# Performance work log

Hardware: AMD Instinct MI355X
Metric: run time of the kernel (lower is better)

Reference implementation:

```python
import jax, jax.numpy as jnp
import numpy as np
import math

B, T, D = 16, 4, 1024
H = 16
DH = D // H  # 64
S = 8192  # kv cache length


def setup_inputs() -> dict:
    key = jax.random.key(0)
    ks = jax.random.split(key, 5)
    return {
        "x": jax.random.normal(ks[0], (B, T, D), dtype=jnp.float32),
        "cache_k": jax.random.normal(ks[1], (B, S, H, DH), dtype=jnp.float32),
        "cache_v": jax.random.normal(ks[2], (B, S, H, DH), dtype=jnp.float32),
        "w_qkv": jax.random.normal(ks[3], (3 * D, D), dtype=jnp.float32) * 0.02,
        "w_proj": jax.random.normal(ks[4], (D, D), dtype=jnp.float32) * (0.02 / math.sqrt(24)),
    }


def reference(x, cache_k, cache_v, w_qkv, w_proj):
    # QKV projection: [B,T,3D]
    qkv = jnp.einsum('btd,ed->bte', x, w_qkv)
    q, k, v = jnp.split(qkv, 3, axis=-1)
    q = q.reshape(B, T, H, DH)
    k = k.reshape(B, T, H, DH)
    v = v.reshape(B, T, H, DH)
    # KV cache concat along sequence dim
    k = jnp.concatenate([cache_k, k], axis=1)  # [B,S+T,H,DH]
    v = jnp.concatenate([cache_v, v], axis=1)
    # scaled dot-product attention (no mask, dropout=0)
    scores = jnp.einsum('bthd,bshd->bhts', q, k) / math.sqrt(DH)
    attn = jax.nn.softmax(scores.astype(jnp.float32), axis=-1).astype(q.dtype)
    out = jnp.einsum('bhts,bshd->bthd', attn, v).reshape(B, T, D)
    # output projection
    out = jnp.einsum('btd,ed->bte', out, w_proj)
    return out
```

## Files before the change

### kernel.cpp

```cpp
#include <hip/hip_runtime.h>
#include <math.h>

#define B_ 16
#define T_ 4
#define D_ 1024
#define H_ 16
#define DH_ 64
#define S_ 8192
#define NW 8
#define ROWS_PER_WAVE (S_ / NW)
#define UNROLL 4

__device__ __forceinline__ void online_step(const float4* q4, const float4& kf,
                                            const float4& vf, float* m, float* l,
                                            float4* o) {
  float sc[T_];
#pragma unroll
  for (int t = 0; t < T_; ++t)
    sc[t] = q4[t].x * kf.x + q4[t].y * kf.y + q4[t].z * kf.z + q4[t].w * kf.w;
#pragma unroll
  for (int mask = 1; mask < 16; mask <<= 1) {
#pragma unroll
    for (int t = 0; t < T_; ++t) sc[t] += __shfl_xor(sc[t], mask);
  }
#pragma unroll
  for (int t = 0; t < T_; ++t) {
    float s = sc[t] * 0.125f;
    float nm = fmaxf(m[t], s);
    float al = __expf(m[t] - nm);
    float p = __expf(s - nm);
    m[t] = nm;
    l[t] = fmaf(l[t], al, p);
    o[t].x = fmaf(o[t].x, al, p * vf.x);
    o[t].y = fmaf(o[t].y, al, p * vf.y);
    o[t].z = fmaf(o[t].z, al, p * vf.z);
    o[t].w = fmaf(o[t].w, al, p * vf.w);
  }
}

__device__ __forceinline__ void merge_xor(int mask, float* m, float* l, float4* o) {
#pragma unroll
  for (int t = 0; t < T_; ++t) {
    float om = __shfl_xor(m[t], mask);
    float ol = __shfl_xor(l[t], mask);
    float4 oo;
    oo.x = __shfl_xor(o[t].x, mask);
    oo.y = __shfl_xor(o[t].y, mask);
    oo.z = __shfl_xor(o[t].z, mask);
    oo.w = __shfl_xor(o[t].w, mask);
    float nm = fmaxf(m[t], om);
    float ea = __expf(m[t] - nm);
    float eb = __expf(om - nm);
    m[t] = nm;
    l[t] = l[t] * ea + ol * eb;
    o[t].x = o[t].x * ea + oo.x * eb;
    o[t].y = o[t].y * ea + oo.y * eb;
    o[t].z = o[t].z * ea + oo.z * eb;
    o[t].w = o[t].w * ea + oo.w * eb;
  }
}

__global__ __launch_bounds__(NW * 64) void attn_kernel(
    const float* __restrict__ qkv, const float* __restrict__ cache_k,
    const float* __restrict__ cache_v, float* __restrict__ attn_out) {
  const int bh = blockIdx.x;
  const int b = bh >> 4;
  const int h = bh & 15;
  const int tid = threadIdx.x;
  const int wave = tid >> 6;
  const int lane = tid & 63;
  const int s_sub = lane >> 4;
  const int d4 = lane & 15;

  float4 q4[T_];
#pragma unroll
  for (int t = 0; t < T_; ++t)
    q4[t] = *(const float4*)(qkv + (size_t)((b * T_ + t) * 3 * D_ + h * DH_ + d4 * 4));

  const float* kbase = cache_k + (size_t)b * S_ * D_ + h * DH_ + d4 * 4;
  const float* vbase = cache_v + (size_t)b * S_ * D_ + h * DH_ + d4 * 4;

  float m[T_], l[T_];
  float4 o[T_];
#pragma unroll
  for (int t = 0; t < T_; ++t) {
    m[t] = -1e30f;
    l[t] = 0.f;
    o[t] = make_float4(0.f, 0.f, 0.f, 0.f);
  }

  const int row0 = wave * ROWS_PER_WAVE + s_sub;
  for (int it = 0; it < ROWS_PER_WAVE / (4 * UNROLL); ++it) {
    const float* kp = kbase + (size_t)(row0 + it * 4 * UNROLL) * D_;
    const float* vp = vbase + (size_t)(row0 + it * 4 * UNROLL) * D_;
    float4 kf[UNROLL], vf[UNROLL];
#pragma unroll
    for (int u = 0; u < UNROLL; ++u) {
      kf[u] = *(const float4*)(kp + (size_t)u * 4 * D_);
      vf[u] = *(const float4*)(vp + (size_t)u * 4 * D_);
    }
#pragma unroll
    for (int u = 0; u < UNROLL; ++u) online_step(q4, kf[u], vf[u], m, l, o);
  }

  if (wave == 0) {
    const float* krow = qkv + (size_t)((b * T_ + s_sub) * 3 * D_ + D_ + h * DH_ + d4 * 4);
    const float* vrow = qkv + (size_t)((b * T_ + s_sub) * 3 * D_ + 2 * D_ + h * DH_ + d4 * 4);
    float4 kf = *(const float4*)krow;
    float4 vf = *(const float4*)vrow;
    online_step(q4, kf, vf, m, l, o);
  }

  merge_xor(16, m, l, o);
  merge_xor(32, m, l, o);

  __shared__ float lm[NW][T_];
  __shared__ float ll[NW][T_];
  __shared__ float lo[NW][T_][DH_];
  if (lane < 16) {
#pragma unroll
    for (int t = 0; t < T_; ++t) {
      if (lane == 0) {
        lm[wave][t] = m[t];
        ll[wave][t] = l[t];
      }
      *(float4*)(&lo[wave][t][lane * 4]) = o[t];
    }
  }
  __syncthreads();
  if (tid < DH_) {
    const int d = tid;
#pragma unroll
    for (int t = 0; t < T_; ++t) {
      float M = -1e30f;
#pragma unroll
      for (int w = 0; w < NW; ++w) M = fmaxf(M, lm[w][t]);
      float L = 0.f, O = 0.f;
#pragma unroll
      for (int w = 0; w < NW; ++w) {
        float e = __expf(lm[w][t] - M);
        L += ll[w][t] * e;
        O += lo[w][t][d] * e;
      }
      attn_out[(size_t)(b * T_ + t) * D_ + h * DH_ + d] = O / L;
    }
  }
}

__global__ __launch_bounds__(256) void gemm_xwt(const float* __restrict__ A,
                                                const float* __restrict__ W,
                                                float* __restrict__ C, int N) {
  const int K = 1024;
  __shared__ float As[32][65];
  __shared__ float Bs[32][65];
  const int tid = threadIdx.x;
  const int n0 = blockIdx.x * 64;
  const int tx = tid & 15;
  const int ty = tid >> 4;
  const int lrow = tid >> 2;
  const int lk = (tid & 3) * 8;

  float acc[4][4] = {};
  for (int k0 = 0; k0 < K; k0 += 32) {
    float4 a0 = *(const float4*)(A + (size_t)lrow * K + k0 + lk);
    float4 a1 = *(const float4*)(A + (size_t)lrow * K + k0 + lk + 4);
    float4 b0 = *(const float4*)(W + (size_t)(n0 + lrow) * K + k0 + lk);
    float4 b1 = *(const float4*)(W + (size_t)(n0 + lrow) * K + k0 + lk + 4);
    As[lk + 0][lrow] = a0.x; As[lk + 1][lrow] = a0.y;
    As[lk + 2][lrow] = a0.z; As[lk + 3][lrow] = a0.w;
    As[lk + 4][lrow] = a1.x; As[lk + 5][lrow] = a1.y;
    As[lk + 6][lrow] = a1.z; As[lk + 7][lrow] = a1.w;
    Bs[lk + 0][lrow] = b0.x; Bs[lk + 1][lrow] = b0.y;
    Bs[lk + 2][lrow] = b0.z; Bs[lk + 3][lrow] = b0.w;
    Bs[lk + 4][lrow] = b1.x; Bs[lk + 5][lrow] = b1.y;
    Bs[lk + 6][lrow] = b1.z; Bs[lk + 7][lrow] = b1.w;
    __syncthreads();
#pragma unroll
    for (int kk = 0; kk < 32; ++kk) {
      float a[4], bb[4];
#pragma unroll
      for (int i = 0; i < 4; ++i) a[i] = As[kk][ty * 4 + i];
#pragma unroll
      for (int j = 0; j < 4; ++j) bb[j] = Bs[kk][tx * 4 + j];
#pragma unroll
      for (int i = 0; i < 4; ++i)
#pragma unroll
        for (int j = 0; j < 4; ++j) acc[i][j] = fmaf(a[i], bb[j], acc[i][j]);
    }
    __syncthreads();
  }
#pragma unroll
  for (int i = 0; i < 4; ++i)
#pragma unroll
    for (int j = 0; j < 4; ++j)
      C[(size_t)(ty * 4 + i) * N + n0 + tx * 4 + j] = acc[i][j];
}

extern "C" void kernel_launch(void* const* d_in, const int* in_sizes, int n_in,
                              void* d_out, int out_size, void* d_ws, size_t ws_size,
                              hipStream_t stream) {
  const float* x = (const float*)d_in[0];
  const float* cache_k = (const float*)d_in[1];
  const float* cache_v = (const float*)d_in[2];
  const float* w_qkv = (const float*)d_in[3];
  const float* w_proj = (const float*)d_in[4];
  float* out = (float*)d_out;

  float* qkv = (float*)d_ws;
  float* attn = qkv + (size_t)B_ * T_ * 3 * D_;

  gemm_xwt<<<3 * D_ / 64, 256, 0, stream>>>(x, w_qkv, qkv, 3 * D_);
  attn_kernel<<<B_ * H_, NW * 64, 0, stream>>>(qkv, cache_k, cache_v, attn);
  gemm_xwt<<<D_ / 64, 256, 0, stream>>>(attn, w_proj, out, D_);
}
```

Measured before the change: 1.161 ms.

## Split KV sequence across blocks, split-K GEMMs with atomics, exp2 softmax

The attention kernel now splits the 8192-row KV cache into 4 chunks per (batch, head), which quadruples the block count to 1024 and fills more CUs. A new reduce kernel merges the partial (max, sum, output) triples. Both GEMMs use split-K over 8 chunks with atomic adds into pre-zeroed outputs, which also adds parallelism. The softmax folds scale and log2e into q and uses raw v_exp_f32, and processes 4 rows per max/rescale step. Shared-memory reads in the GEMM are vectorised to float4. The cost is two extra launches and nondeterministic float atomics.

New measurement: 1.029 ms. -11.3%, faster.

```diff
diff --git a/kernel.cpp b/kernel.cpp
--- a/kernel.cpp
+++ b/kernel.cpp
@@ -8,27 +8,72 @@
 #define DH_ 64
 #define S_ 8192
 #define NW 8
-#define ROWS_PER_WAVE (S_ / NW)
+#define SPLIT 4
+#define SCH (S_ / SPLIT)
+#define ROWS_PER_WAVE (SCH / NW)
 #define UNROLL 4
-
-__device__ __forceinline__ void online_step(const float4* q4, const float4& kf,
-                                            const float4& vf, float* m, float* l,
-                                            float4* o) {
+#define PSTR 68
+
+__device__ __forceinline__ float exp2_(float x) {
+  float r;
+  asm("v_exp_f32 %0, %1" : "=v"(r) : "v"(x));
+  return r;
+}
+
+__device__ __forceinline__ void online_step4(const float4* q4, const float4* kf,
+                                             const float4* vf, float* m, float* l,
+                                             float4* o) {
+  float sc[UNROLL][T_];
+#pragma unroll
+  for (int u = 0; u < UNROLL; ++u)
+#pragma unroll
+    for (int t = 0; t < T_; ++t)
+      sc[u][t] = q4[t].x * kf[u].x + q4[t].y * kf[u].y + q4[t].z * kf[u].z +
+                 q4[t].w * kf[u].w;
+#pragma unroll
+  for (int mask = 1; mask < 16; mask <<= 1)
+#pragma unroll
+    for (int u = 0; u < UNROLL; ++u)
+#pragma unroll
+      for (int t = 0; t < T_; ++t) sc[u][t] += __shfl_xor(sc[u][t], mask);
+#pragma unroll
+  for (int t = 0; t < T_; ++t) {
+    float nm = fmaxf(fmaxf(sc[0][t], sc[1][t]), fmaxf(sc[2][t], sc[3][t]));
+    nm = fmaxf(nm, m[t]);
+    float al = exp2_(m[t] - nm);
+    float p0 = exp2_(sc[0][t] - nm);
+    float p1 = exp2_(sc[1][t] - nm);
+    float p2 = exp2_(sc[2][t] - nm);
+    float p3 = exp2_(sc[3][t] - nm);
+    m[t] = nm;
+    l[t] = fmaf(l[t], al, (p0 + p1) + (p2 + p3));
+    float ax = p0 * vf[0].x; ax = fmaf(p1, vf[1].x, ax); ax = fmaf(p2, vf[2].x, ax); ax = fmaf(p3, vf[3].x, ax);
+    float ay = p0 * vf[0].y; ay = fmaf(p1, vf[1].y, ay); ay = fmaf(p2, vf[2].y, ay); ay = fmaf(p3, vf[3].y, ay);
+    float az = p0 * vf[0].z; az = fmaf(p1, vf[1].z, az); az = fmaf(p2, vf[2].z, az); az = fmaf(p3, vf[3].z, az);
+    float aw = p0 * vf[0].w; aw = fmaf(p1, vf[1].w, aw); aw = fmaf(p2, vf[2].w, aw); aw = fmaf(p3, vf[3].w, aw);
+    o[t].x = fmaf(o[t].x, al, ax);
+    o[t].y = fmaf(o[t].y, al, ay);
+    o[t].z = fmaf(o[t].z, al, az);
+    o[t].w = fmaf(o[t].w, al, aw);
+  }
+}
+
+__device__ __forceinline__ void online_step1(const float4* q4, const float4& kf,
+                                             const float4& vf, float* m, float* l,
+                                             float4* o) {
   float sc[T_];
 #pragma unroll
   for (int t = 0; t < T_; ++t)
     sc[t] = q4[t].x * kf.x + q4[t].y * kf.y + q4[t].z * kf.z + q4[t].w * kf.w;
 #pragma unroll
-  for (int mask = 1; mask < 16; mask <<= 1) {
+  for (int mask = 1; mask < 16; mask <<= 1)
 #pragma unroll
     for (int t = 0; t < T_; ++t) sc[t] += __shfl_xor(sc[t], mask);
-  }
-#pragma unroll
-  for (int t = 0; t < T_; ++t) {
-    float s = sc[t] * 0.125f;
-    float nm = fmaxf(m[t], s);
-    float al = __expf(m[t] - nm);
-    float p = __expf(s - nm);
+#pragma unroll
+  for (int t = 0; t < T_; ++t) {
+    float nm = fmaxf(m[t], sc[t]);
+    float al = exp2_(m[t] - nm);
+    float p = exp2_(sc[t] - nm);
     m[t] = nm;
     l[t] = fmaf(l[t], al, p);
     o[t].x = fmaf(o[t].x, al, p * vf.x);
@@ -49,8 +94,8 @@
     oo.z = __shfl_xor(o[t].z, mask);
     oo.w = __shfl_xor(o[t].w, mask);
     float nm = fmaxf(m[t], om);
-    float ea = __expf(m[t] - nm);
-    float eb = __expf(om - nm);
+    float ea = exp2_(m[t] - nm);
+    float eb = exp2_(om - nm);
     m[t] = nm;
     l[t] = l[t] * ea + ol * eb;
     o[t].x = o[t].x * ea + oo.x * eb;
@@ -60,10 +105,12 @@
   }
 }
 
-__global__ __launch_bounds__(NW * 64) void attn_kernel(
+__global__ __launch_bounds__(NW * 64, 4) void attn_kernel(
     const float* __restrict__ qkv, const float* __restrict__ cache_k,
-    const float* __restrict__ cache_v, float* __restrict__ attn_out) {
-  const int bh = blockIdx.x;
+    const float* __restrict__ cache_v, float* __restrict__ part) {
+  const int blk = blockIdx.x;
+  const int bh = blk >> 2;
+  const int split = blk & 3;
   const int b = bh >> 4;
   const int h = bh & 15;
   const int tid = threadIdx.x;
@@ -72,10 +119,13 @@
   const int s_sub = lane >> 4;
   const int d4 = lane & 15;
 
+  const float qs = 0.125f * 1.44269504088896340736f;
   float4 q4[T_];
 #pragma unroll
-  for (int t = 0; t < T_; ++t)
-    q4[t] = *(const float4*)(qkv + (size_t)((b * T_ + t) * 3 * D_ + h * DH_ + d4 * 4));
+  for (int t = 0; t < T_; ++t) {
+    float4 q = *(const float4*)(qkv + (size_t)((b * T_ + t) * 3 * D_ + h * DH_ + d4 * 4));
+    q4[t] = make_float4(q.x * qs, q.y * qs, q.z * qs, q.w * qs);
+  }
 
   const float* kbase = cache_k + (size_t)b * S_ * D_ + h * DH_ + d4 * 4;
   const float* vbase = cache_v + (size_t)b * S_ * D_ + h * DH_ + d4 * 4;
@@ -89,7 +139,7 @@
     o[t] = make_float4(0.f, 0.f, 0.f, 0.f);
   }
 
-  const int row0 = wave * ROWS_PER_WAVE + s_sub;
+  const int row0 = split * SCH + wave * ROWS_PER_WAVE + s_sub;
   for (int it = 0; it < ROWS_PER_WAVE / (4 * UNROLL); ++it) {
     const float* kp = kbase + (size_t)(row0 + it * 4 * UNROLL) * D_;
     const float* vp = vbase + (size_t)(row0 + it * 4 * UNROLL) * D_;
@@ -99,16 +149,15 @@
       kf[u] = *(const float4*)(kp + (size_t)u * 4 * D_);
       vf[u] = *(const float4*)(vp + (size_t)u * 4 * D_);
     }
-#pragma unroll
-    for (int u = 0; u < UNROLL; ++u) online_step(q4, kf[u], vf[u], m, l, o);
-  }
-
-  if (wave == 0) {
+    online_step4(q4, kf, vf, m, l, o);
+  }
+
+  if (split == SPLIT - 1 && wave == 0) {
     const float* krow = qkv + (size_t)((b * T_ + s_sub) * 3 * D_ + D_ + h * DH_ + d4 * 4);
     const float* vrow = qkv + (size_t)((b * T_ + s_sub) * 3 * D_ + 2 * D_ + h * DH_ + d4 * 4);
     float4 kf = *(const float4*)krow;
     float4 vf = *(const float4*)vrow;
-    online_step(q4, kf, vf, m, l, o);
+    online_step1(q4, kf, vf, m, l, o);
   }
 
   merge_xor(16, m, l, o);
@@ -129,39 +178,76 @@
   }
   __syncthreads();
   if (tid < DH_) {
-    const int d = tid;
 #pragma unroll
     for (int t = 0; t < T_; ++t) {
-      float M = -1e30f;
-#pragma unroll
-      for (int w = 0; w < NW; ++w) M = fmaxf(M, lm[w][t]);
+      float M = lm[0][t];
+#pragma unroll
+      for (int w = 1; w < NW; ++w) M = fmaxf(M, lm[w][t]);
       float L = 0.f, O = 0.f;
 #pragma unroll
       for (int w = 0; w < NW; ++w) {
-        float e = __expf(lm[w][t] - M);
-        L += ll[w][t] * e;
-        O += lo[w][t][d] * e;
+        float e = exp2_(lm[w][t] - M);
+        L = fmaf(ll[w][t], e, L);
+        O = fmaf(lo[w][t][tid], e, O);
       }
-      attn_out[(size_t)(b * T_ + t) * D_ + h * DH_ + d] = O / L;
-    }
-  }
+      float* pp = part + ((size_t)blk * T_ + t) * PSTR;
+      pp[tid] = O;
+      if (tid == 0) {
+        pp[DH_] = M;
+        pp[DH_ + 1] = L;
+      }
+    }
+  }
+}
+
+__global__ __launch_bounds__(64) void attn_reduce(const float* __restrict__ part,
+                                                  float* __restrict__ attn_out,
+                                                  float4* __restrict__ out_zero) {
+  const int bh = blockIdx.x;
+  const int b = bh >> 4;
+  const int h = bh & 15;
+  const int d = threadIdx.x;
+  out_zero[(size_t)bh * DH_ + d] = make_float4(0.f, 0.f, 0.f, 0.f);
+#pragma unroll
+  for (int t = 0; t < T_; ++t) {
+    const float* p0 = part + ((size_t)(bh * SPLIT) * T_ + t) * PSTR;
+    float M = p0[DH_];
+#pragma unroll
+    for (int sp = 1; sp < SPLIT; ++sp)
+      M = fmaxf(M, p0[(size_t)sp * T_ * PSTR + DH_]);
+    float L = 0.f, O = 0.f;
+#pragma unroll
+    for (int sp = 0; sp < SPLIT; ++sp) {
+      const float* pp = p0 + (size_t)sp * T_ * PSTR;
+      float e = exp2_(pp[DH_] - M);
+      L = fmaf(pp[DH_ + 1], e, L);
+      O = fmaf(pp[d], e, O);
+    }
+    attn_out[(size_t)(b * T_ + t) * D_ + h * DH_ + d] = O / L;
+  }
+}
+
+__global__ __launch_bounds__(256) void zero4(float4* __restrict__ p) {
+  p[(size_t)blockIdx.x * 256 + threadIdx.x] = make_float4(0.f, 0.f, 0.f, 0.f);
 }
 
 __global__ __launch_bounds__(256) void gemm_xwt(const float* __restrict__ A,
                                                 const float* __restrict__ W,
-                                                float* __restrict__ C, int N) {
+                                                float* __restrict__ C, int N,
+                                                int KCH) {
   const int K = 1024;
-  __shared__ float As[32][65];
-  __shared__ float Bs[32][65];
+  __shared__ float As[32][68];
+  __shared__ float Bs[32][68];
   const int tid = threadIdx.x;
   const int n0 = blockIdx.x * 64;
+  const int kb = blockIdx.y * KCH;
   const int tx = tid & 15;
   const int ty = tid >> 4;
   const int lrow = tid >> 2;
   const int lk = (tid & 3) * 8;
 
   float acc[4][4] = {};
-  for (int k0 = 0; k0 < K; k0 += 32) {
+  for (int k0 = kb; k0 < kb + KCH; k0 += 32) {
     float4 a0 = *(const float4*)(A + (size_t)lrow * K + k0 + lk);
     float4 a1 = *(const float4*)(A + (size_t)lrow * K + k0 + lk + 4);
     float4 b0 = *(const float4*)(W + (size_t)(n0 + lrow) * K + k0 + lk);
@@ -177,11 +263,10 @@
     __syncthreads();
 #pragma unroll
     for (int kk = 0; kk < 32; ++kk) {
-      float a[4], bb[4];
-#pragma unroll
-      for (int i = 0; i < 4; ++i) a[i] = As[kk][ty * 4 + i];
-#pragma unroll
-      for (int j = 0; j < 4; ++j) bb[j] = Bs[kk][tx * 4 + j];
+      const float4 av = *(const float4*)&As[kk][ty * 4];
+      const float4 bv = *(const float4*)&Bs[kk][tx * 4];
+      const float a[4] = {av.x, av.y, av.z, av.w};
+      const float bb[4] = {bv.x, bv.y, bv.z, bv.w};
 #pragma unroll
       for (int i = 0; i < 4; ++i)
 #pragma unroll
@@ -193,7 +278,7 @@
   for (int i = 0; i < 4; ++i)
 #pragma unroll
     for (int j = 0; j < 4; ++j)
-      C[(size_t)(ty * 4 + i) * N + n0 + tx * 4 + j] = acc[i][j];
+      unsafeAtomicAdd(&C[(size_t)(ty * 4 + i) * N + n0 + tx * 4 + j], acc[i][j]);
 }
 
 extern "C" void kernel_launch(void* const* d_in, const int* in_sizes, int n_in,
@@ -208,8 +293,11 @@
 
   float* qkv = (float*)d_ws;
   float* attn = qkv + (size_t)B_ * T_ * 3 * D_;
-
-  gemm_xwt<<<3 * D_ / 64, 256, 0, stream>>>(x, w_qkv, qkv, 3 * D_);
-  attn_kernel<<<B_ * H_, NW * 64, 0, stream>>>(qkv, cache_k, cache_v, attn);
-  gemm_xwt<<<D_ / 64, 256, 0, stream>>>(attn, w_proj, out, D_);
-}
+  float* part = attn + (size_t)B_ * T_ * D_;
+
+  zero4<<<192, 256, 0, stream>>>((float4*)qkv);
+  gemm_xwt<<<dim3(3 * D_ / 64, 8), 256, 0, stream>>>(x, w_qkv, qkv, 3 * D_, 128);
+  attn_kernel<<<B_ * H_ * SPLIT, NW * 64, 0, stream>>>(qkv, cache_k, cache_v, part);
+  attn_reduce<<<B_ * H_, 64, 0, stream>>>(part, attn, (float4*)out);
+  gemm_xwt<<<dim3(D_ / 64, 8), 256, 0, stream>>>(attn, w_proj, out, D_, 128);
+}
```
